# Optimization experiments

Measured on AMD Instinct MI355X. Metric: run time of the kernel, lower is better.

The kernel has to match this reference:

```python
import jax, jax.numpy as jnp
import numpy as np

N_NODES = 20000
N_EDGES = 160000
N_CONFIG = 1000
OP_SIZE = 120
OP_FEATURE = 140
CONFIG_FEATURE = 24
HID = 256
EMB = 128


def _mynorm(x, axis):
    # InstanceNorm1d (affine=False): biased var, eps=1e-5, normalized over `axis`
    m = jnp.mean(x, axis=axis, keepdims=True)
    v = jnp.var(x, axis=axis, keepdims=True)
    return (x - m) / jnp.sqrt(v + 1e-5)


def _gelu(x):
    return jax.nn.gelu(x, approximate=False)


def _segment_softmax(e, seg, num):
    m = jax.ops.segment_max(e, seg, num_segments=num)
    ex = jnp.exp(e - m[seg])
    s = jax.ops.segment_sum(ex, seg, num_segments=num)
    return ex / (s[seg] + 1e-16)


def setup_inputs() -> dict:
    key = jax.random.key(0)
    ks = jax.random.split(key, 24)
    d = {}
    d['node_feat'] = jax.random.normal(ks[0], (N_NODES, OP_FEATURE), jnp.float32)
    d['config_feat'] = jax.random.normal(ks[1], (N_CONFIG, CONFIG_FEATURE), jnp.float32)
    d['node_feat_mean'] = jax.random.normal(ks[2], (OP_FEATURE,), jnp.float32)
    d['node_feat_std'] = jax.random.uniform(ks[3], (OP_FEATURE,), jnp.float32)
    d['config_feat_mean'] = jax.random.normal(ks[4], (CONFIG_FEATURE,), jnp.float32)
    d['config_feat_std'] = jax.random.uniform(ks[5], (CONFIG_FEATURE,), jnp.float32)
    d['embed_table'] = jax.random.normal(ks[6], (OP_SIZE, EMB), jnp.float32)
    d['early_W1'] = jax.random.normal(ks[7], (EMB + OP_FEATURE, HID), jnp.float32) * 0.05
    d['early_W2'] = jax.random.normal(ks[8], (HID, HID), jnp.float32) * 0.05
    d['gat_Wl'] = jax.random.normal(ks[9], (4, HID, HID), jnp.float32) * 0.05
    d['gat_bl'] = jax.random.normal(ks[10], (4, HID), jnp.float32) * 0.05
    d['gat_Wr'] = jax.random.normal(ks[11], (4, HID, HID), jnp.float32) * 0.05
    d['gat_br'] = jax.random.normal(ks[12], (4, HID), jnp.float32) * 0.05
    d['gat_att'] = jax.random.normal(ks[13], (4, HID), jnp.float32) * 0.05
    d['gat_bias'] = jax.random.normal(ks[14], (4, HID), jnp.float32) * 0.05
    d['late_W1'] = jax.random.normal(ks[15], (HID + CONFIG_FEATURE, HID), jnp.float32) * 0.05
    d['late_W2'] = jax.random.normal(ks[16], (HID, HID // 2), jnp.float32) * 0.05
    d['pred_W'] = jax.random.normal(ks[17], (HID // 2, 1), jnp.float32) * 0.05
    d['pred_b'] = jax.random.normal(ks[18], (1,), jnp.float32) * 0.05
    d['node_opcode'] = jax.random.randint(ks[19], (N_NODES,), 0, OP_SIZE, jnp.int64)
    d['edge_index'] = jax.random.randint(ks[20], (2, N_EDGES), 0, N_NODES, jnp.int64)
    return d


def reference(node_feat, config_feat, node_feat_mean, node_feat_std,
              config_feat_mean, config_feat_std, embed_table,
              early_W1, early_W2, gat_Wl, gat_bl, gat_Wr, gat_br,
              gat_att, gat_bias, late_W1, late_W2, pred_W, pred_b,
              node_opcode, edge_index):
    N = node_feat.shape[0]
    # embedding with max_norm=1: renormalize looked-up rows to L2 norm <= 1
    emb = embed_table[node_opcode]
    nrm = jnp.sqrt(jnp.sum(emb * emb, axis=-1, keepdims=True))
    emb = emb * jnp.minimum(1.0, 1.0 / (nrm + 1e-7))
    feat = (node_feat - node_feat_mean) / (node_feat_std + 1e-4)
    x = jnp.concatenate([emb, feat], axis=-1)  # [N, 268]
    # early MLP (norm over node axis per channel)
    x = _gelu(_mynorm(x @ early_W1, 0))
    x = _gelu(_mynorm(x @ early_W2, 0))
    # add self loops (PyG GATv2Conv default)
    loop = jnp.arange(N, dtype=edge_index.dtype)
    src = jnp.concatenate([edge_index[0], loop])  # message source j
    dst = jnp.concatenate([edge_index[1], loop])  # message target i
    for i in range(4):
        xl = x @ gat_Wl[i] + gat_bl[i]
        xr = x @ gat_Wr[i] + gat_br[i]
        h = xl[src] + xr[dst]                      # [E+N, HID]
        e = jax.nn.leaky_relu(h, 0.2) @ gat_att[i]  # [E+N]
        alpha = _segment_softmax(e, dst, N)
        out = jax.ops.segment_sum(alpha[:, None] * xl[src], dst, num_segments=N)
        out = out + gat_bias[i]
        x = _gelu(_mynorm(out, 0))
    pool = jnp.mean(x, axis=0) + jnp.max(x, axis=0)  # [HID]
    cf = (config_feat - config_feat_mean) / (config_feat_std + 1e-4)
    C = cf.shape[0]
    x_late = jnp.concatenate([cf, jnp.broadcast_to(pool, (C, pool.shape[0]))], axis=1)
    h = _gelu(_mynorm(x_late @ late_W1, 0))  # 2D MyNorm1d normalizes over batch axis
    h = _gelu(_mynorm(h @ late_W2, 0))
    runtime = (h @ pred_W + pred_b)[:, 0]
    return runtime
```

## Files before the change

kernel.cpp:

```cpp
#include <hip/hip_runtime.h>
#include <math.h>

#define N_NODES 20000
#define N_EDGES 160000
#define N_CFG   1000
#define OP_FEAT 140
#define CFG_FEAT 24
#define HID     256
#define EMB     128
#define E_TOT   (N_EDGES + N_NODES)
#define K288    288
#define MPAD    20096
#define NW      512

typedef __attribute__((ext_vector_type(8))) short short8v;
typedef __attribute__((ext_vector_type(4))) float f32x4;

__device__ __forceinline__ short f2bf(float f) {
  unsigned u = __float_as_uint(f);
  unsigned r = (u + 0x7FFFu + ((u >> 16) & 1u)) >> 16;
  return (short)r;
}
__device__ __forceinline__ float bf2f(short s) {
  return __uint_as_float(((unsigned)(unsigned short)s) << 16);
}
__device__ __forceinline__ float gelu_f(float x) {
  return 0.5f * x * (1.0f + erff(x * 0.70710678118654752f));
}

#define GLOAD_LDS(gptr, lptr) __builtin_amdgcn_global_load_lds( \
    (const __attribute__((address_space(1))) void*)(gptr),      \
    (__attribute__((address_space(3))) void*)(lptr), 16, 0, 0)

__global__ void convert_wt(const float* __restrict__ W, short* __restrict__ Wt,
                           int K, int N, int Kpad)
{
  int i = blockIdx.x * blockDim.x + threadIdx.x;
  if (i >= N * Kpad) return;
  int n = i / Kpad, k = i % Kpad;
  Wt[i] = (k < K) ? f2bf(W[(size_t)k * N + n]) : (short)0;
}

__global__ void gat_wt_prep(const float* __restrict__ Wl, const float* __restrict__ Wr,
                            short* __restrict__ dst)
{
  int i = blockIdx.x * blockDim.x + threadIdx.x;
  if (i >= 4 * NW * HID) return;
  int l = i >> 17, rem = i & 131071;
  int n = rem >> 8, k = rem & 255;
  float v = (n < HID) ? Wl[(size_t)l * HID * HID + (size_t)k * HID + n]
                      : Wr[(size_t)l * HID * HID + (size_t)k * HID + (n - HID)];
  dst[i] = f2bf(v);
}

__global__ void bias_cat(const float* __restrict__ bl, const float* __restrict__ br,
                         float* __restrict__ blr)
{
  int i = blockIdx.x * blockDim.x + threadIdx.x;
  if (i >= 4 * NW) return;
  int l = i >> 9, j = i & 511;
  blr[i] = (j < HID) ? bl[l * HID + j] : br[l * HID + j - HID];
}

__global__ __launch_bounds__(256) void prep_kernel(
    const float* __restrict__ node_feat, const float* __restrict__ nf_mean,
    const float* __restrict__ nf_std, const float* __restrict__ emb_table,
    const int* __restrict__ opcode, short* __restrict__ x268b)
{
  int wave = threadIdx.x >> 6;
  int lane = threadIdx.x & 63;
  int row = blockIdx.x * 4 + wave;
  if (row >= N_NODES) return;
  int op = opcode[row];
  float t0 = emb_table[op * EMB + lane];
  float t1 = emb_table[op * EMB + 64 + lane];
  float ss = t0 * t0 + t1 * t1;
  #pragma unroll
  for (int off = 32; off; off >>= 1) ss += __shfl_xor(ss, off);
  float sc = fminf(1.0f, 1.0f / (sqrtf(ss) + 1e-7f));
  short* dst = x268b + (size_t)row * K288;
  dst[lane] = f2bf(t0 * sc);
  dst[64 + lane] = f2bf(t1 * sc);
  for (int k = lane; k < OP_FEAT; k += 64)
    dst[EMB + k] = f2bf((node_feat[(size_t)row * OP_FEAT + k] - nf_mean[k]) / (nf_std[k] + 1e-4f));
  if (lane < K288 - EMB - OP_FEAT) dst[EMB + OP_FEAT + lane] = 0;
}

__global__ __launch_bounds__(256) void gemm_mfma(
    const short* __restrict__ A, const short* __restrict__ Wt,
    const float* __restrict__ bias, float* __restrict__ C,
    int M, int N, int Kpad)
{
  __shared__ __align__(16) short As[4][128][8];
  __shared__ __align__(16) short Bs[4][128][8];
  int tid = threadIdx.x;
  int wave = tid >> 6, lane = tid & 63;
  int bm = blockIdx.x * 128, bn = blockIdx.y * 128;
  int wr = (wave >> 1) * 64, wc = (wave & 1) * 64;
  int g = lane >> 4, r16 = lane & 15;
  f32x4 acc[4][4] = {};

  for (int k0 = 0; k0 < Kpad; k0 += 32) {
    #pragma unroll
    for (int s2 = 0; s2 < 2; s2++) {
      int s = wave * 2 + s2;
      int sg = s >> 1, r0 = (s & 1) * 64;
      GLOAD_LDS(A  + (size_t)(bm + r0 + lane) * Kpad + k0 + sg * 8, &As[sg][r0][0]);
      GLOAD_LDS(Wt + (size_t)(bn + r0 + lane) * Kpad + k0 + sg * 8, &Bs[sg][r0][0]);
    }
    __syncthreads();
    short8v af[4], bfv[4];
    #pragma unroll
    for (int mi = 0; mi < 4; mi++)
      af[mi] = *(const short8v*)&As[g][wr + mi * 16 + r16][0];
    #pragma unroll
    for (int ni = 0; ni < 4; ni++)
      bfv[ni] = *(const short8v*)&Bs[g][wc + ni * 16 + r16][0];
    #pragma unroll
    for (int mi = 0; mi < 4; mi++)
      #pragma unroll
      for (int ni = 0; ni < 4; ni++)
        acc[mi][ni] = __builtin_amdgcn_mfma_f32_16x16x32_bf16(af[mi], bfv[ni], acc[mi][ni], 0, 0, 0);
    __syncthreads();
  }

  int rg = lane >> 4;
  #pragma unroll
  for (int mi = 0; mi < 4; mi++) {
    #pragma unroll
    for (int r = 0; r < 4; r++) {
      int gr = bm + wr + mi * 16 + rg * 4 + r;
      if (gr >= M) continue;
      #pragma unroll
      for (int ni = 0; ni < 4; ni++) {
        int gc = bn + wc + ni * 16 + r16;
        float v = acc[mi][ni][r];
        if (bias) v += bias[gc];
        C[(size_t)gr * N + gc] = v;
      }
    }
  }
}

__global__ void colstats(const float* __restrict__ X, int M, int C,
                         float* __restrict__ stats)
{
  int c = threadIdx.x;
  int r0 = blockIdx.x * 64;
  int r1 = min(r0 + 64, M);
  float s = 0.f, sq = 0.f;
  for (int r = r0; r < r1; r++) {
    float v = X[(size_t)r * C + c];
    s += v; sq += v * v;
  }
  atomicAdd(&stats[c], s);
  atomicAdd(&stats[C + c], sq);
}

__global__ void norm_gelu(const float* __restrict__ X, float* __restrict__ Yf,
                          short* __restrict__ Yb, int M, int C,
                          const float* __restrict__ stats)
{
  int i = blockIdx.x * blockDim.x + threadIdx.x;
  if (i >= M * C) return;
  int c = i % C;
  float invM = 1.0f / (float)M;
  float mean = stats[c] * invM;
  float var = stats[C + c] * invM - mean * mean;
  float y = gelu_f((X[i] - mean) * rsqrtf(var + 1e-5f));
  if (Yf) Yf[i] = y;
  if (Yb) Yb[i] = f2bf(y);
}

__global__ void edge_count(const int* __restrict__ ei, int* __restrict__ counts) {
  int e = blockIdx.x * blockDim.x + threadIdx.x;
  if (e >= E_TOT) return;
  int dst = (e < N_EDGES) ? ei[N_EDGES + e] : (e - N_EDGES);
  atomicAdd(&counts[dst], 1);
}

__global__ __launch_bounds__(1024) void scan_kernel(const int* __restrict__ counts,
                                                    int* __restrict__ indptr)
{
  __shared__ int sh[1024];
  int t = threadIdx.x;
  const int chunk = (N_NODES + 1023) / 1024;
  int start = t * chunk, end = min(start + chunk, N_NODES);
  int sum = 0;
  for (int i = start; i < end; i++) sum += counts[i];
  sh[t] = sum;
  __syncthreads();
  for (int off = 1; off < 1024; off <<= 1) {
    int v = (t >= off) ? sh[t - off] : 0;
    __syncthreads();
    sh[t] += v;
    __syncthreads();
  }
  int run = (t > 0) ? sh[t - 1] : 0;
  for (int i = start; i < end; i++) { indptr[i] = run; run += counts[i]; }
  if (t == 1023) indptr[N_NODES] = run;
}

__global__ void edge_fill(const int* __restrict__ ei, const int* __restrict__ indptr,
                          int* __restrict__ cursor, int* __restrict__ col)
{
  int e = blockIdx.x * blockDim.x + threadIdx.x;
  if (e >= E_TOT) return;
  int src, dst;
  if (e < N_EDGES) { src = ei[e]; dst = ei[N_EDGES + e]; }
  else             { src = dst = e - N_EDGES; }
  int pos = indptr[dst] + atomicAdd(&cursor[dst], 1);
  col[pos] = src;
}

__global__ __launch_bounds__(256) void gat_agg(
    const float* __restrict__ xlr,
    const int* __restrict__ indptr, const int* __restrict__ col,
    const float* __restrict__ att, const float* __restrict__ bias,
    float* __restrict__ out)
{
  int wave = threadIdx.x >> 6, lane = threadIdx.x & 63;
  int node = blockIdx.x * 4 + wave;
  if (node >= N_NODES) return;
  float attc[4], xri[4], o[4] = {0, 0, 0, 0};
  #pragma unroll
  for (int k = 0; k < 4; k++) {
    attc[k] = att[lane + 64 * k];
    xri[k] = xlr[(size_t)node * NW + HID + lane + 64 * k];
  }
  float m = -INFINITY, s = 0.f;
  int e0 = indptr[node], e1 = indptr[node + 1];
  for (int e = e0; e < e1; e++) {
    int j = col[e];
    float xlj[4], p = 0.f;
    #pragma unroll
    for (int k = 0; k < 4; k++) {
      xlj[k] = xlr[(size_t)j * NW + lane + 64 * k];
      float h = xlj[k] + xri[k];
      float lr = h > 0.f ? h : 0.2f * h;
      p += lr * attc[k];
    }
    #pragma unroll
    for (int off = 32; off; off >>= 1) p += __shfl_xor(p, off);
    float mn = fmaxf(m, p);
    float scale = __expf(m - mn);
    float w = __expf(p - mn);
    s = s * scale + w;
    #pragma unroll
    for (int k = 0; k < 4; k++) o[k] = o[k] * scale + w * xlj[k];
    m = mn;
  }
  float inv = 1.0f / (s + 1e-16f);
  #pragma unroll
  for (int k = 0; k < 4; k++)
    out[(size_t)node * HID + lane + 64 * k] = o[k] * inv + bias[lane + 64 * k];
}

__device__ __forceinline__ unsigned fenc(float f) {
  unsigned b = __float_as_uint(f);
  return (b & 0x80000000u) ? ~b : (b | 0x80000000u);
}
__device__ __forceinline__ float fdec(unsigned u) {
  unsigned b = (u & 0x80000000u) ? (u & 0x7FFFFFFFu) : ~u;
  return __uint_as_float(b);
}

__global__ void pool_reduce(const short* __restrict__ Xb, float* __restrict__ psum,
                            unsigned* __restrict__ pmax)
{
  int c = threadIdx.x;
  int r0 = blockIdx.x * 64, r1 = min(r0 + 64, N_NODES);
  float s = 0.f, mx = -INFINITY;
  for (int r = r0; r < r1; r++) {
    float v = bf2f(Xb[(size_t)r * HID + c]);
    s += v; mx = fmaxf(mx, v);
  }
  atomicAdd(&psum[c], s);
  atomicMax(&pmax[c], fenc(mx));
}

__global__ void pool_finalize(const float* __restrict__ psum,
                              const unsigned* __restrict__ pmax,
                              float* __restrict__ pool)
{
  int c = threadIdx.x;
  pool[c] = psum[c] * (1.0f / N_NODES) + fdec(pmax[c]);
}

__global__ void build_xlate(const float* __restrict__ cfg, const float* __restrict__ cmean,
                            const float* __restrict__ cstd, const float* __restrict__ pool,
                            short* __restrict__ xlateb)
{
  int i = blockIdx.x * blockDim.x + threadIdx.x;
  if (i >= N_CFG * K288) return;
  int r = i / K288, c = i % K288;
  float v;
  if (c < CFG_FEAT) v = (cfg[r * CFG_FEAT + c] - cmean[c]) / (cstd[c] + 1e-4f);
  else if (c < CFG_FEAT + HID) v = pool[c - CFG_FEAT];
  else v = 0.f;
  xlateb[i] = f2bf(v);
}

__global__ __launch_bounds__(64) void pred_kernel(
    const float* __restrict__ h2, const float* __restrict__ W,
    const float* __restrict__ b, float* __restrict__ out)
{
  int r = blockIdx.x, lane = threadIdx.x;
  float v = h2[(size_t)r * 128 + lane] * W[lane] +
            h2[(size_t)r * 128 + 64 + lane] * W[64 + lane];
  #pragma unroll
  for (int off = 32; off; off >>= 1) v += __shfl_xor(v, off);
  if (lane == 0) out[r] = v + b[0];
}

extern "C" void kernel_launch(void* const* d_in, const int* in_sizes, int n_in,
                              void* d_out, int out_size, void* d_ws, size_t ws_size,
                              hipStream_t stream)
{
  const float* node_feat   = (const float*)d_in[0];
  const float* config_feat = (const float*)d_in[1];
  const float* nf_mean     = (const float*)d_in[2];
  const float* nf_std      = (const float*)d_in[3];
  const float* cf_mean     = (const float*)d_in[4];
  const float* cf_std      = (const float*)d_in[5];
  const float* emb_table   = (const float*)d_in[6];
  const float* early_W1    = (const float*)d_in[7];
  const float* early_W2    = (const float*)d_in[8];
  const float* gat_Wl      = (const float*)d_in[9];
  const float* gat_bl      = (const float*)d_in[10];
  const float* gat_Wr      = (const float*)d_in[11];
  const float* gat_br      = (const float*)d_in[12];
  const float* gat_att     = (const float*)d_in[13];
  const float* gat_bias    = (const float*)d_in[14];
  const float* late_W1     = (const float*)d_in[15];
  const float* late_W2     = (const float*)d_in[16];
  const float* pred_W      = (const float*)d_in[17];
  const float* pred_b      = (const float*)d_in[18];
  const int*   node_opcode = (const int*)d_in[19];
  const int*   edge_index  = (const int*)d_in[20];
  float* out = (float*)d_out;
  (void)in_sizes; (void)n_in; (void)out_size; (void)ws_size;

  char* ws = (char*)d_ws;
  size_t off = 0;
  auto alloc = [&](size_t bytes) -> void* {
    void* p = ws + off;
    off += (bytes + 255) & ~255ull;
    return p;
  };
  short* x268b = (short*)alloc((size_t)MPAD * K288 * 2);
  float* bufB  = (float*)alloc((size_t)N_NODES * HID * 4);
  short* bufAb = (short*)alloc((size_t)MPAD * HID * 2);
  float* xlr   = (float*)alloc((size_t)N_NODES * NW * 4);
  float* stats = (float*)alloc(2 * HID * 4);
  int* counts  = (int*)alloc(N_NODES * 4);
  int* indptr  = (int*)alloc((N_NODES + 1) * 4);
  int* colidx  = (int*)alloc((size_t)E_TOT * 4);
  float* psum  = (float*)alloc(HID * 4);
  unsigned* pmax = (unsigned*)alloc(HID * 4);
  float* pool  = (float*)alloc(HID * 4);
  short* xlateb = (short*)alloc((size_t)1024 * K288 * 2);
  float* h1    = (float*)alloc((size_t)N_CFG * HID * 4);
  short* h1b   = (short*)alloc((size_t)1024 * HID * 2);
  float* h2    = (float*)alloc((size_t)N_CFG * 128 * 4);
  float* h2n   = (float*)alloc((size_t)N_CFG * 128 * 4);
  short* W1t   = (short*)alloc((size_t)HID * K288 * 2);
  short* W2t   = (short*)alloc((size_t)HID * HID * 2);
  short* Wlrt  = (short*)alloc((size_t)4 * NW * HID * 2);
  float* blr   = (float*)alloc(4 * NW * 4);
  short* lW1t  = (short*)alloc((size_t)HID * K288 * 2);
  short* lW2t  = (short*)alloc((size_t)128 * HID * 2);

  auto run_gemm = [&](const short* A, const short* Wt, const float* bias, float* C,
                      int M, int N, int Kpad) {
    dim3 grid((M + 127) / 128, N / 128);
    hipLaunchKernelGGL(gemm_mfma, grid, dim3(256), 0, stream, A, Wt, bias, C, M, N, Kpad);
  };
  auto run_norm = [&](const float* X, float* Yf, short* Yb, int M, int C) {
    hipMemsetAsync(stats, 0, 2 * C * sizeof(float), stream);
    hipLaunchKernelGGL(colstats, dim3((M + 63) / 64), dim3(C), 0, stream, X, M, C, stats);
    hipLaunchKernelGGL(norm_gelu, dim3((M * C + 255) / 256), dim3(256), 0, stream,
                       X, Yf, Yb, M, C, stats);
  };

  hipLaunchKernelGGL(convert_wt, dim3((HID * K288 + 255) / 256), dim3(256), 0, stream,
                     early_W1, W1t, EMB + OP_FEAT, HID, K288);
  hipLaunchKernelGGL(convert_wt, dim3((HID * HID + 255) / 256), dim3(256), 0, stream,
                     early_W2, W2t, HID, HID, HID);
  hipLaunchKernelGGL(convert_wt, dim3((HID * K288 + 255) / 256), dim3(256), 0, stream,
                     late_W1, lW1t, CFG_FEAT + HID, HID, K288);
  hipLaunchKernelGGL(convert_wt, dim3((128 * HID + 255) / 256), dim3(256), 0, stream,
                     late_W2, lW2t, HID, 128, HID);
  hipLaunchKernelGGL(gat_wt_prep, dim3((4 * NW * HID + 255) / 256), dim3(256), 0, stream,
                     gat_Wl, gat_Wr, Wlrt);
  hipLaunchKernelGGL(bias_cat, dim3((4 * NW + 255) / 256), dim3(256), 0, stream,
                     gat_bl, gat_br, blr);

  hipMemsetAsync(counts, 0, N_NODES * 4, stream);
  hipLaunchKernelGGL(edge_count, dim3((E_TOT + 255) / 256), dim3(256), 0, stream,
                     edge_index, counts);
  hipLaunchKernelGGL(scan_kernel, dim3(1), dim3(1024), 0, stream, counts, indptr);
  hipMemsetAsync(counts, 0, N_NODES * 4, stream);
  hipLaunchKernelGGL(edge_fill, dim3((E_TOT + 255) / 256), dim3(256), 0, stream,
                     edge_index, indptr, counts, colidx);

  hipLaunchKernelGGL(prep_kernel, dim3((N_NODES + 3) / 4), dim3(256), 0, stream,
                     node_feat, nf_mean, nf_std, emb_table, node_opcode, x268b);
  run_gemm(x268b, W1t, nullptr, bufB, N_NODES, HID, K288);
  run_norm(bufB, nullptr, bufAb, N_NODES, HID);
  run_gemm(bufAb, W2t, nullptr, bufB, N_NODES, HID, HID);
  run_norm(bufB, nullptr, bufAb, N_NODES, HID);

  for (int l = 0; l < 4; l++) {
    run_gemm(bufAb, Wlrt + (size_t)l * NW * HID, blr + l * NW, xlr, N_NODES, NW, HID);
    hipLaunchKernelGGL(gat_agg, dim3((N_NODES + 3) / 4), dim3(256), 0, stream,
                       xlr, indptr, colidx, gat_att + l * HID, gat_bias + l * HID, bufB);
    run_norm(bufB, nullptr, bufAb, N_NODES, HID);
  }

  hipMemsetAsync(psum, 0, HID * 4, stream);
  hipMemsetAsync(pmax, 0, HID * 4, stream);
  hipLaunchKernelGGL(pool_reduce, dim3((N_NODES + 63) / 64), dim3(HID), 0, stream,
                     bufAb, psum, pmax);
  hipLaunchKernelGGL(pool_finalize, dim3(1), dim3(HID), 0, stream, psum, pmax, pool);

  hipLaunchKernelGGL(build_xlate, dim3((N_CFG * K288 + 255) / 256), dim3(256), 0, stream,
                     config_feat, cf_mean, cf_std, pool, xlateb);
  run_gemm(xlateb, lW1t, nullptr, h1, N_CFG, HID, K288);
  run_norm(h1, nullptr, h1b, N_CFG, HID);
  run_gemm(h1b, lW2t, nullptr, h2, N_CFG, 128, HID);
  run_norm(h2, h2n, nullptr, N_CFG, 128);
  hipLaunchKernelGGL(pred_kernel, dim3(N_CFG), dim3(64), 0, stream, h2n, pred_W, pred_b, out);
}
```

Measured before the change: 674.6 us.

## Fuse column statistics into GEMM epilogue and merge prep launches and memsets

The GEMM epilogue now accumulates per-column sum and sum-of-squares and atomically adds them into a stats slot. This removes the separate colstats pass over the 20000x256 output for the early and late MLP layers. The six weight-prep kernels are merged into one launch, the many memsets become a single zeroing of a combined buffer with one stats slot per layer, and pool_finalize is folded into build_xlate. The final norm+gelu is folded into pred_kernel. In exchange, the GEMM epilogue does more shuffles and atomics, and computing variance from sums in fp32 can lose precision.

```diff
diff --git a/kernel.cpp b/kernel.cpp
--- a/kernel.cpp
+++ b/kernel.cpp
@@ -32,34 +32,41 @@
     (const __attribute__((address_space(1))) void*)(gptr),      \
     (__attribute__((address_space(3))) void*)(lptr), 16, 0, 0)
 
-__global__ void convert_wt(const float* __restrict__ W, short* __restrict__ Wt,
-                           int K, int N, int Kpad)
-{
-  int i = blockIdx.x * blockDim.x + threadIdx.x;
-  if (i >= N * Kpad) return;
-  int n = i / Kpad, k = i % Kpad;
-  Wt[i] = (k < K) ? f2bf(W[(size_t)k * N + n]) : (short)0;
-}
-
-__global__ void gat_wt_prep(const float* __restrict__ Wl, const float* __restrict__ Wr,
-                            short* __restrict__ dst)
-{
-  int i = blockIdx.x * blockDim.x + threadIdx.x;
-  if (i >= 4 * NW * HID) return;
-  int l = i >> 17, rem = i & 131071;
-  int n = rem >> 8, k = rem & 255;
-  float v = (n < HID) ? Wl[(size_t)l * HID * HID + (size_t)k * HID + n]
-                      : Wr[(size_t)l * HID * HID + (size_t)k * HID + (n - HID)];
-  dst[i] = f2bf(v);
-}
-
-__global__ void bias_cat(const float* __restrict__ bl, const float* __restrict__ br,
-                         float* __restrict__ blr)
-{
-  int i = blockIdx.x * blockDim.x + threadIdx.x;
-  if (i >= 4 * NW) return;
-  int l = i >> 9, j = i & 511;
-  blr[i] = (j < HID) ? bl[l * HID + j] : br[l * HID + j - HID];
+__global__ void prep_weights(
+    const float* __restrict__ eW1, const float* __restrict__ eW2,
+    const float* __restrict__ lW1, const float* __restrict__ lW2,
+    const float* __restrict__ Wl, const float* __restrict__ Wr,
+    const float* __restrict__ bl, const float* __restrict__ br,
+    short* __restrict__ W1t, short* __restrict__ W2t,
+    short* __restrict__ lW1t, short* __restrict__ lW2t,
+    short* __restrict__ Wlrt, float* __restrict__ blr)
+{
+  int i = blockIdx.x * 256 + threadIdx.x;
+  const int s1 = HID * K288;
+  const int s2 = HID * HID;
+  const int s3 = HID * K288;
+  const int s4 = 128 * HID;
+  const int s5 = 4 * NW * HID;
+  const int s6 = 4 * NW;
+  if (i < s1) { int n = i / K288, k = i % K288;
+    W1t[i] = (k < EMB + OP_FEAT) ? f2bf(eW1[(size_t)k * HID + n]) : (short)0; return; }
+  i -= s1;
+  if (i < s2) { int n = i >> 8, k = i & 255;
+    W2t[i] = f2bf(eW2[(size_t)k * HID + n]); return; }
+  i -= s2;
+  if (i < s3) { int n = i / K288, k = i % K288;
+    lW1t[i] = (k < CFG_FEAT + HID) ? f2bf(lW1[(size_t)k * HID + n]) : (short)0; return; }
+  i -= s3;
+  if (i < s4) { int n = i >> 8, k = i & 255;
+    lW2t[i] = f2bf(lW2[(size_t)k * 128 + n]); return; }
+  i -= s4;
+  if (i < s5) { int l = i >> 17, rem = i & 131071, n = rem >> 8, k = rem & 255;
+    float v = (n < HID) ? Wl[(size_t)l * HID * HID + (size_t)k * HID + n]
+                        : Wr[(size_t)l * HID * HID + (size_t)k * HID + (n - HID)];
+    Wlrt[i] = f2bf(v); return; }
+  i -= s5;
+  if (i < s6) { int l = i >> 9, j = i & 511;
+    blr[i] = (j < HID) ? bl[l * HID + j] : br[l * HID + j - HID]; }
 }
 
 __global__ __launch_bounds__(256) void prep_kernel(
@@ -89,7 +96,7 @@
 __global__ __launch_bounds__(256) void gemm_mfma(
     const short* __restrict__ A, const short* __restrict__ Wt,
     const float* __restrict__ bias, float* __restrict__ C,
-    int M, int N, int Kpad)
+    float* __restrict__ stats, int M, int N, int Kpad)
 {
   __shared__ __align__(16) short As[4][128][8];
   __shared__ __align__(16) short Bs[4][128][8];
@@ -126,18 +133,26 @@
 
   int rg = lane >> 4;
   #pragma unroll
-  for (int mi = 0; mi < 4; mi++) {
-    #pragma unroll
-    for (int r = 0; r < 4; r++) {
-      int gr = bm + wr + mi * 16 + rg * 4 + r;
-      if (gr >= M) continue;
+  for (int ni = 0; ni < 4; ni++) {
+    int gc = bn + wc + ni * 16 + r16;
+    float bv = bias ? bias[gc] : 0.f;
+    float s = 0.f, sq = 0.f;
+    #pragma unroll
+    for (int mi = 0; mi < 4; mi++) {
       #pragma unroll
-      for (int ni = 0; ni < 4; ni++) {
-        int gc = bn + wc + ni * 16 + r16;
-        float v = acc[mi][ni][r];
-        if (bias) v += bias[gc];
-        C[(size_t)gr * N + gc] = v;
+      for (int r = 0; r < 4; r++) {
+        int gr = bm + wr + mi * 16 + rg * 4 + r;
+        if (gr < M) {
+          float v = acc[mi][ni][r] + bv;
+          C[(size_t)gr * N + gc] = v;
+          s += v; sq += v * v;
+        }
       }
+    }
+    if (stats) {
+      s  += __shfl_xor(s, 16);  sq += __shfl_xor(sq, 16);
+      s  += __shfl_xor(s, 32);  sq += __shfl_xor(sq, 32);
+      if (rg == 0) { atomicAdd(&stats[gc], s); atomicAdd(&stats[N + gc], sq); }
     }
   }
 }
@@ -157,9 +172,8 @@
   atomicAdd(&stats[C + c], sq);
 }
 
-__global__ void norm_gelu(const float* __restrict__ X, float* __restrict__ Yf,
-                          short* __restrict__ Yb, int M, int C,
-                          const float* __restrict__ stats)
+__global__ void norm_gelu(const float* __restrict__ X, short* __restrict__ Yb,
+                          int M, int C, const float* __restrict__ stats)
 {
   int i = blockIdx.x * blockDim.x + threadIdx.x;
   if (i >= M * C) return;
@@ -168,8 +182,7 @@
   float mean = stats[c] * invM;
   float var = stats[C + c] * invM - mean * mean;
   float y = gelu_f((X[i] - mean) * rsqrtf(var + 1e-5f));
-  if (Yf) Yf[i] = y;
-  if (Yb) Yb[i] = f2bf(y);
+  Yb[i] = f2bf(y);
 }
 
 __global__ void edge_count(const int* __restrict__ ei, int* __restrict__ counts) {
@@ -279,35 +292,38 @@
   atomicMax(&pmax[c], fenc(mx));
 }
 
-__global__ void pool_finalize(const float* __restrict__ psum,
-                              const unsigned* __restrict__ pmax,
-                              float* __restrict__ pool)
-{
-  int c = threadIdx.x;
-  pool[c] = psum[c] * (1.0f / N_NODES) + fdec(pmax[c]);
-}
-
 __global__ void build_xlate(const float* __restrict__ cfg, const float* __restrict__ cmean,
-                            const float* __restrict__ cstd, const float* __restrict__ pool,
-                            short* __restrict__ xlateb)
+                            const float* __restrict__ cstd, const float* __restrict__ psum,
+                            const unsigned* __restrict__ pmax, short* __restrict__ xlateb)
 {
   int i = blockIdx.x * blockDim.x + threadIdx.x;
   if (i >= N_CFG * K288) return;
   int r = i / K288, c = i % K288;
   float v;
   if (c < CFG_FEAT) v = (cfg[r * CFG_FEAT + c] - cmean[c]) / (cstd[c] + 1e-4f);
-  else if (c < CFG_FEAT + HID) v = pool[c - CFG_FEAT];
-  else v = 0.f;
+  else if (c < CFG_FEAT + HID) {
+    int p = c - CFG_FEAT;
+    v = psum[p] * (1.0f / N_NODES) + fdec(pmax[p]);
+  } else v = 0.f;
   xlateb[i] = f2bf(v);
 }
 
 __global__ __launch_bounds__(64) void pred_kernel(
-    const float* __restrict__ h2, const float* __restrict__ W,
-    const float* __restrict__ b, float* __restrict__ out)
+    const float* __restrict__ h2, const float* __restrict__ stats,
+    const float* __restrict__ W, const float* __restrict__ b,
+    float* __restrict__ out)
 {
   int r = blockIdx.x, lane = threadIdx.x;
-  float v = h2[(size_t)r * 128 + lane] * W[lane] +
-            h2[(size_t)r * 128 + 64 + lane] * W[64 + lane];
+  const float invM = 1.0f / (float)N_CFG;
+  float v = 0.f;
+  #pragma unroll
+  for (int t = 0; t < 2; t++) {
+    int c = lane + 64 * t;
+    float mean = stats[c] * invM;
+    float var = stats[128 + c] * invM - mean * mean;
+    float y = gelu_f((h2[(size_t)r * 128 + c] - mean) * rsqrtf(var + 1e-5f));
+    v += y * W[c];
+  }
   #pragma unroll
   for (int off = 32; off; off >>= 1) v += __shfl_xor(v, off);
   if (lane == 0) out[r] = v + b[0];
@@ -352,18 +368,12 @@
   float* bufB  = (float*)alloc((size_t)N_NODES * HID * 4);
   short* bufAb = (short*)alloc((size_t)MPAD * HID * 2);
   float* xlr   = (float*)alloc((size_t)N_NODES * NW * 4);
-  float* stats = (float*)alloc(2 * HID * 4);
-  int* counts  = (int*)alloc(N_NODES * 4);
   int* indptr  = (int*)alloc((N_NODES + 1) * 4);
   int* colidx  = (int*)alloc((size_t)E_TOT * 4);
-  float* psum  = (float*)alloc(HID * 4);
-  unsigned* pmax = (unsigned*)alloc(HID * 4);
-  float* pool  = (float*)alloc(HID * 4);
   short* xlateb = (short*)alloc((size_t)1024 * K288 * 2);
   float* h1    = (float*)alloc((size_t)N_CFG * HID * 4);
   short* h1b   = (short*)alloc((size_t)1024 * HID * 2);
   float* h2    = (float*)alloc((size_t)N_CFG * 128 * 4);
-  float* h2n   = (float*)alloc((size_t)N_CFG * 128 * 4);
   short* W1t   = (short*)alloc((size_t)HID * K288 * 2);
   short* W2t   = (short*)alloc((size_t)HID * HID * 2);
   short* Wlrt  = (short*)alloc((size_t)4 * NW * HID * 2);
@@ -371,64 +381,64 @@
   short* lW1t  = (short*)alloc((size_t)HID * K288 * 2);
   short* lW2t  = (short*)alloc((size_t)128 * HID * 2);
 
+  float* zbase = (float*)alloc((8 * 1024 + 512 + 2 * N_NODES) * 4);
+  float* stats8 = zbase;
+  float* psum   = zbase + 8192;
+  unsigned* pmax = (unsigned*)(zbase + 8192 + 256);
+  int* counts   = (int*)(zbase + 8192 + 512);
+  int* cursor   = counts + N_NODES;
+  const size_t zbytes = (8 * 1024 + 512 + 2 * N_NODES) * 4;
+  auto slot = [&](int s) { return stats8 + s * 1024; };
+
   auto run_gemm = [&](const short* A, const short* Wt, const float* bias, float* C,
-                      int M, int N, int Kpad) {
+                      float* stats, int M, int N, int Kpad) {
     dim3 grid((M + 127) / 128, N / 128);
-    hipLaunchKernelGGL(gemm_mfma, grid, dim3(256), 0, stream, A, Wt, bias, C, M, N, Kpad);
+    hipLaunchKernelGGL(gemm_mfma, grid, dim3(256), 0, stream, A, Wt, bias, C, stats, M, N, Kpad);
   };
-  auto run_norm = [&](const float* X, float* Yf, short* Yb, int M, int C) {
-    hipMemsetAsync(stats, 0, 2 * C * sizeof(float), stream);
-    hipLaunchKernelGGL(colstats, dim3((M + 63) / 64), dim3(C), 0, stream, X, M, C, stats);
-    hipLaunchKernelGGL(norm_gelu, dim3((M * C + 255) / 256), dim3(256), 0, stream,
-                       X, Yf, Yb, M, C, stats);
-  };
-
-  hipLaunchKernelGGL(convert_wt, dim3((HID * K288 + 255) / 256), dim3(256), 0, stream,
-                     early_W1, W1t, EMB + OP_FEAT, HID, K288);
-  hipLaunchKernelGGL(convert_wt, dim3((HID * HID + 255) / 256), dim3(256), 0, stream,
-                     early_W2, W2t, HID, HID, HID);
-  hipLaunchKernelGGL(convert_wt, dim3((HID * K288 + 255) / 256), dim3(256), 0, stream,
-                     late_W1, lW1t, CFG_FEAT + HID, HID, K288);
-  hipLaunchKernelGGL(convert_wt, dim3((128 * HID + 255) / 256), dim3(256), 0, stream,
-                     late_W2, lW2t, HID, 128, HID);
-  hipLaunchKernelGGL(gat_wt_prep, dim3((4 * NW * HID + 255) / 256), dim3(256), 0, stream,
-                     gat_Wl, gat_Wr, Wlrt);
-  hipLaunchKernelGGL(bias_cat, dim3((4 * NW + 255) / 256), dim3(256), 0, stream,
-                     gat_bl, gat_br, blr);
-
-  hipMemsetAsync(counts, 0, N_NODES * 4, stream);
+
+  hipMemsetAsync(zbase, 0, zbytes, stream);
+
+  {
+    int total = HID * K288 + HID * HID + HID * K288 + 128 * HID + 4 * NW * HID + 4 * NW;
+    hipLaunchKernelGGL(prep_weights, dim3((total + 255) / 256), dim3(256), 0, stream,
+                       early_W1, early_W2, late_W1, late_W2, gat_Wl, gat_Wr, gat_bl, gat_br,
+                       W1t, W2t, lW1t, lW2t, Wlrt, blr);
+  }
+
   hipLaunchKernelGGL(edge_count, dim3((E_TOT + 255) / 256), dim3(256), 0, stream,
                      edge_index, counts);
   hipLaunchKernelGGL(scan_kernel, dim3(1), dim3(1024), 0, stream, counts, indptr);
-  hipMemsetAsync(counts, 0, N_NODES * 4, stream);
   hipLaunchKernelGGL(edge_fill, dim3((E_TOT + 255) / 256), dim3(256), 0, stream,
-                     edge_index, indptr, counts, colidx);
+                     edge_index, indptr, cursor, colidx);
 
   hipLaunchKernelGGL(prep_kernel, dim3((N_NODES + 3) / 4), dim3(256), 0, stream,
                      node_feat, nf_mean, nf_std, emb_table, node_opcode, x268b);
-  run_gemm(x268b, W1t, nullptr, bufB, N_NODES, HID, K288);
-  run_norm(bufB, nullptr, bufAb, N_NODES, HID);
-  run_gemm(bufAb, W2t, nullptr, bufB, N_NODES, HID, HID);
-  run_norm(bufB, nullptr, bufAb, N_NODES, HID);
+  run_gemm(x268b, W1t, nullptr, bufB, slot(0), N_NODES, HID, K288);
+  hipLaunchKernelGGL(norm_gelu, dim3((N_NODES * HID + 255) / 256), dim3(256), 0, stream,
+                     bufB, bufAb, N_NODES, HID, slot(0));
+  run_gemm(bufAb, W2t, nullptr, bufB, slot(1), N_NODES, HID, HID);
+  hipLaunchKernelGGL(norm_gelu, dim3((N_NODES * HID + 255) / 256), dim3(256), 0, stream,
+                     bufB, bufAb, N_NODES, HID, slot(1));
 
   for (int l = 0; l < 4; l++) {
-    run_gemm(bufAb, Wlrt + (size_t)l * NW * HID, blr + l * NW, xlr, N_NODES, NW, HID);
+    run_gemm(bufAb, Wlrt + (size_t)l * NW * HID, blr + l * NW, xlr, nullptr, N_NODES, NW, HID);
     hipLaunchKernelGGL(gat_agg, dim3((N_NODES + 3) / 4), dim3(256), 0, stream,
                        xlr, indptr, colidx, gat_att + l * HID, gat_bias + l * HID, bufB);
-    run_norm(bufB, nullptr, bufAb, N_NODES, HID);
-  }
-
-  hipMemsetAsync(psum, 0, HID * 4, stream);
-  hipMemsetAsync(pmax, 0, HID * 4, stream);
+    hipLaunchKernelGGL(colstats, dim3((N_NODES + 63) / 64), dim3(HID), 0, stream,
+                       bufB, N_NODES, HID, slot(2 + l));
+    hipLaunchKernelGGL(norm_gelu, dim3((N_NODES * HID + 255) / 256), dim3(256), 0, stream,
+                       bufB, bufAb, N_NODES, HID, slot(2 + l));
+  }
+
   hipLaunchKernelGGL(pool_reduce, dim3((N_NODES + 63) / 64), dim3(HID), 0, stream,
                      bufAb, psum, pmax);
-  hipLaunchKernelGGL(pool_finalize, dim3(1), dim3(HID), 0, stream, psum, pmax, pool);
 
   hipLaunchKernelGGL(build_xlate, dim3((N_CFG * K288 + 255) / 256), dim3(256), 0, stream,
-                     config_feat, cf_mean, cf_std, pool, xlateb);
-  run_gemm(xlateb, lW1t, nullptr, h1, N_CFG, HID, K288);
-  run_norm(h1, nullptr, h1b, N_CFG, HID);
-  run_gemm(h1b, lW2t, nullptr, h2, N_CFG, 128, HID);
-  run_norm(h2, h2n, nullptr, N_CFG, 128);
-  hipLaunchKernelGGL(pred_kernel, dim3(N_CFG), dim3(64), 0, stream, h2n, pred_W, pred_b, out);
-}
+                     config_feat, cf_mean, cf_std, psum, pmax, xlateb);
+  run_gemm(xlateb, lW1t, nullptr, h1, slot(6), N_CFG, HID, K288);
+  hipLaunchKernelGGL(norm_gelu, dim3((N_CFG * HID + 255) / 256), dim3(256), 0, stream,
+                     h1, h1b, N_CFG, HID, slot(6));
+  run_gemm(h1b, lW2t, nullptr, h2, slot(7), N_CFG, 128, HID);
+  hipLaunchKernelGGL(pred_kernel, dim3(N_CFG), dim3(64), 0, stream,
+                     h2, slot(7), pred_W, pred_b, out);
+}
```

After: 601.1 us. 10.9% less time.
